# Optimization experiments

Hardware: AMD Instinct MI355X
Metric: run time of the kernel (lower is better)

## Reference

```python
import jax, jax.numpy as jnp
import numpy as np

POOL = (7, 7)


def crop_and_resize(image, boxes, box_idx, crop_size):
    """Faithful jnp port of tf.image.crop_and_resize (bilinear, extrapolation_value=0).

    image: [B, H, W, C]; boxes: [N, 4] normalized (y1, x1, y2, x2); box_idx: [N] int.
    Returns [N, ph, pw, C].
    """
    H, W = image.shape[1], image.shape[2]
    ph, pw = crop_size
    y1, x1, y2, x2 = boxes[:, 0], boxes[:, 1], boxes[:, 2], boxes[:, 3]
    iy = jnp.arange(ph, dtype=image.dtype)
    ix = jnp.arange(pw, dtype=image.dtype)
    # sample coords in source-pixel space, TF convention for crop_size > 1
    ys = y1[:, None] * (H - 1) + iy[None, :] * ((y2 - y1)[:, None] * (H - 1) / (ph - 1))  # [N, ph]
    xs = x1[:, None] * (W - 1) + ix[None, :] * ((x2 - x1)[:, None] * (W - 1) / (pw - 1))  # [N, pw]
    vy = (ys >= 0) & (ys <= H - 1)
    vx = (xs >= 0) & (xs <= W - 1)
    y0 = jnp.floor(ys)
    x0 = jnp.floor(xs)
    wy = (ys - y0)[:, :, None, None]   # [N, ph, 1, 1]
    wx = (xs - x0)[:, None, :, None]   # [N, 1, pw, 1]
    y0i = jnp.clip(y0, 0, H - 1).astype(jnp.int32)
    y1i = jnp.clip(y0 + 1, 0, H - 1).astype(jnp.int32)  # when ys is integral, wy==0 so clamp is harmless
    x0i = jnp.clip(x0, 0, W - 1).astype(jnp.int32)
    x1i = jnp.clip(x0 + 1, 0, W - 1).astype(jnp.int32)
    b = box_idx[:, None, None]

    def g(yi, xi):
        return image[b, yi[:, :, None], xi[:, None, :], :]  # [N, ph, pw, C]

    top = g(y0i, x0i) * (1 - wx) + g(y0i, x1i) * wx
    bot = g(y1i, x0i) * (1 - wx) + g(y1i, x1i) * wx
    out = top * (1 - wy) + bot * wy
    valid = (vy[:, :, None] & vx[:, None, :])[..., None]
    return jnp.where(valid, out, jnp.zeros((), image.dtype))


def setup_inputs() -> dict:
    key = jax.random.key(0)
    kb, kp, k3, k4, k5 = jax.random.split(key, 5)
    B, N, C = 2, 1000, 256
    # valid normalized boxes: per-axis sorted uniforms -> y1 <= y2, x1 <= x2
    raw = jax.random.uniform(kb, (B, N, 2, 2), dtype=jnp.float32)  # [..., (y|x), (lo,hi)]
    raw = jnp.sort(raw, axis=-1)
    boxes = jnp.stack([raw[..., 0, 0], raw[..., 1, 0], raw[..., 0, 1], raw[..., 1, 1]], axis=-1)
    return {
        "boxes": boxes,
        "positive_indices": jax.random.randint(kp, (B, N), 0, 2, dtype=jnp.int32),
        "p3": jax.random.normal(k3, (B, 128, 128, C), dtype=jnp.float32),
        "p4": jax.random.normal(k4, (B, 64, 64, C), dtype=jnp.float32),
        "p5": jax.random.normal(k5, (B, 32, 32, C), dtype=jnp.float32),
        "config": 0,
    }


def reference(boxes, positive_indices, p3, p4, p5, config):
    B, N = boxes.shape[0], boxes.shape[1]
    ph, pw = POOL
    h = boxes[..., 2] - boxes[..., 0]
    w = boxes[..., 3] - boxes[..., 1]
    # roi_level = clip(ceil(5 + log2(h*w)), 3, 5); clip in float first (log2(0) -> -inf)
    lvl = jnp.ceil(5.0 + jnp.log(h * w) / jnp.log(2.0))
    roi_level = jnp.clip(lvl, 3.0, 5.0).astype(jnp.int32)  # [B, N]
    boxes_flat = jax.lax.stop_gradient(boxes.reshape(B * N, 4))  # boxes get no grad in original
    lvl_flat = roi_level.reshape(B * N)
    box_idx = jnp.repeat(jnp.arange(B, dtype=jnp.int32), N)
    C = p3.shape[-1]
    pooled = jnp.zeros((B * N, ph, pw, C), dtype=p3.dtype)
    for level, feat in zip((3, 4, 5), (p3, p4, p5)):
        crop = crop_and_resize(feat, boxes_flat, box_idx, POOL)
        mask = (lvl_flat == level)[:, None, None, None]
        pooled = jnp.where(mask, crop, pooled)
    return pooled.reshape(B, N, ph, pw, C)
```

## Files before the change

kernel.cpp:

```cpp
#include <hip/hip_runtime.h>
#include <math.h>


#define NBOX   2000
#define N_PER_B 1000
#define CCH    256
#define PH     7
#define PW     7
#define NPOS   (PH * PW)

__global__ __launch_bounds__(256) void pyramid_roi_align_kernel(
    const float* __restrict__ boxes,
    const float* __restrict__ p3,
    const float* __restrict__ p4,
    const float* __restrict__ p5,
    float* __restrict__ out)
{
    const int tid  = blockIdx.x * blockDim.x + threadIdx.x;
    const int lane = threadIdx.x & 63;
    const int gpos = tid >> 6;
    if (gpos >= NBOX * NPOS) return;

    const int box = gpos / NPOS;
    const int pos = gpos - box * NPOS;
    const int iy  = pos / PW;
    const int ix  = pos - iy * PW;

    const float y1 = boxes[box * 4 + 0];
    const float x1 = boxes[box * 4 + 1];
    const float y2 = boxes[box * 4 + 2];
    const float x2 = boxes[box * 4 + 3];
    const float h  = y2 - y1;
    const float w  = x2 - x1;

    const float lvl = ceilf(5.0f + logf(h * w) / 0.69314718055994530942f);
    const float lvlc = fminf(fmaxf(lvl, 3.0f), 5.0f);
    const int level = (int)lvlc;

    const float* feat;
    int H;
    if (level <= 3)      { feat = p3; H = 128; }
    else if (level == 4) { feat = p4; H = 64;  }
    else                 { feat = p5; H = 32;  }
    const int W = H;

    const int b = (box >= N_PER_B) ? 1 : 0;
    feat += (size_t)b * H * W * CCH;

    const float Hm1 = (float)(H - 1);
    const float Wm1 = (float)(W - 1);

    const float ys = y1 * Hm1 + (float)iy * (h * Hm1 / 6.0f);
    const float xs = x1 * Wm1 + (float)ix * (w * Wm1 / 6.0f);

    const bool vy = (ys >= 0.0f) && (ys <= Hm1);
    const bool vx = (xs >= 0.0f) && (xs <= Wm1);
    const bool valid = vy && vx;

    const float y0f = floorf(ys);
    const float x0f = floorf(xs);
    const float wy  = ys - y0f;
    const float wx  = xs - x0f;

    const int y0i = (int)fminf(fmaxf(y0f,        0.0f), Hm1);
    const int y1i = (int)fminf(fmaxf(y0f + 1.0f, 0.0f), Hm1);
    const int x0i = (int)fminf(fmaxf(x0f,        0.0f), Wm1);
    const int x1i = (int)fminf(fmaxf(x0f + 1.0f, 0.0f), Wm1);

    const int c = lane * 4;
    const float4* r00 = (const float4*)(feat + ((size_t)(y0i * W + x0i)) * CCH + c);
    const float4* r01 = (const float4*)(feat + ((size_t)(y0i * W + x1i)) * CCH + c);
    const float4* r10 = (const float4*)(feat + ((size_t)(y1i * W + x0i)) * CCH + c);
    const float4* r11 = (const float4*)(feat + ((size_t)(y1i * W + x1i)) * CCH + c);

    const float4 v00 = *r00;
    const float4 v01 = *r01;
    const float4 v10 = *r10;
    const float4 v11 = *r11;

    const float omwx = 1.0f - wx;
    const float omwy = 1.0f - wy;

    float4 res;
    {
        const float t0 = v00.x * omwx + v01.x * wx;
        const float b0 = v10.x * omwx + v11.x * wx;
        res.x = t0 * omwy + b0 * wy;
        const float t1 = v00.y * omwx + v01.y * wx;
        const float b1 = v10.y * omwx + v11.y * wx;
        res.y = t1 * omwy + b1 * wy;
        const float t2 = v00.z * omwx + v01.z * wx;
        const float b2 = v10.z * omwx + v11.z * wx;
        res.z = t2 * omwy + b2 * wy;
        const float t3 = v00.w * omwx + v01.w * wx;
        const float b3 = v10.w * omwx + v11.w * wx;
        res.w = t3 * omwy + b3 * wy;
    }

    if (!valid) { res.x = 0.0f; res.y = 0.0f; res.z = 0.0f; res.w = 0.0f; }

    float4* dst = (float4*)(out + (size_t)gpos * CCH + c);
    *dst = res;
}

extern "C" void kernel_launch(void* const* d_in, const int* in_sizes, int n_in,
                              void* d_out, int out_size, void* d_ws, size_t ws_size,
                              hipStream_t stream) {
    const float* boxes = (const float*)d_in[0];
    const float* p3 = (const float*)d_in[2];
    const float* p4 = (const float*)d_in[3];
    const float* p5 = (const float*)d_in[4];
    float* out = (float*)d_out;

    const int total_threads = NBOX * NPOS * 64;
    const int block = 256;
    const int grid = (total_threads + block - 1) / block;

    hipLaunchKernelGGL(pyramid_roi_align_kernel, dim3(grid), dim3(block), 0, stream,
                       boxes, p3, p4, p5, out);
}
```

Baseline: 171.8 us.

## Map one block per box and loop output columns within each wavefront

The kernel now launches one 448-thread block per box, with each of the 7 wavefronts handling one output row and looping over the 7 columns. Box loading, level selection and the row-dependent interpolation terms are computed once per row instead of once per output position. The cost is fewer, longer-running threads and a serial unrolled loop over columns. Occupancy depends on register use under the new launch bounds.

```diff
diff --git a/kernel.cpp b/kernel.cpp
--- a/kernel.cpp
+++ b/kernel.cpp
@@ -2,29 +2,23 @@
 #include <math.h>
 
 
-#define NBOX   2000
 #define N_PER_B 1000
-#define CCH    256
-#define PH     7
-#define PW     7
-#define NPOS   (PH * PW)
+#define NBOX    2000
+#define CCH     256
+#define PH      7
+#define PW      7
 
-__global__ __launch_bounds__(256) void pyramid_roi_align_kernel(
+__global__ __launch_bounds__(448, 4) void pyramid_roi_align_kernel(
     const float* __restrict__ boxes,
     const float* __restrict__ p3,
     const float* __restrict__ p4,
     const float* __restrict__ p5,
     float* __restrict__ out)
 {
-    const int tid  = blockIdx.x * blockDim.x + threadIdx.x;
+    const int box  = blockIdx.x;
+    const int iy   = threadIdx.x >> 6;
     const int lane = threadIdx.x & 63;
-    const int gpos = tid >> 6;
-    if (gpos >= NBOX * NPOS) return;
-
-    const int box = gpos / NPOS;
-    const int pos = gpos - box * NPOS;
-    const int iy  = pos / PW;
-    const int ix  = pos - iy * PW;
+    const int c    = lane * 4;
 
     const float y1 = boxes[box * 4 + 0];
     const float x1 = boxes[box * 4 + 1];
@@ -33,9 +27,9 @@
     const float h  = y2 - y1;
     const float w  = x2 - x1;
 
-    const float lvl = ceilf(5.0f + logf(h * w) / 0.69314718055994530942f);
+    const float lvl  = ceilf(5.0f + logf(h * w) / 0.69314718055994530942f);
     const float lvlc = fminf(fmaxf(lvl, 3.0f), 5.0f);
-    const int level = (int)lvlc;
+    const int level  = (int)lvlc;
 
     const float* feat;
     int H;
@@ -51,56 +45,48 @@
     const float Wm1 = (float)(W - 1);
 
     const float ys = y1 * Hm1 + (float)iy * (h * Hm1 / 6.0f);
-    const float xs = x1 * Wm1 + (float)ix * (w * Wm1 / 6.0f);
-
-    const bool vy = (ys >= 0.0f) && (ys <= Hm1);
-    const bool vx = (xs >= 0.0f) && (xs <= Wm1);
-    const bool valid = vy && vx;
+    const bool  vy = (ys >= 0.0f) && (ys <= Hm1);
 
     const float y0f = floorf(ys);
-    const float x0f = floorf(xs);
     const float wy  = ys - y0f;
-    const float wx  = xs - x0f;
+    const float omwy = 1.0f - wy;
 
     const int y0i = (int)fminf(fmaxf(y0f,        0.0f), Hm1);
     const int y1i = (int)fminf(fmaxf(y0f + 1.0f, 0.0f), Hm1);
-    const int x0i = (int)fminf(fmaxf(x0f,        0.0f), Wm1);
-    const int x1i = (int)fminf(fmaxf(x0f + 1.0f, 0.0f), Wm1);
 
-    const int c = lane * 4;
-    const float4* r00 = (const float4*)(feat + ((size_t)(y0i * W + x0i)) * CCH + c);
-    const float4* r01 = (const float4*)(feat + ((size_t)(y0i * W + x1i)) * CCH + c);
-    const float4* r10 = (const float4*)(feat + ((size_t)(y1i * W + x0i)) * CCH + c);
-    const float4* r11 = (const float4*)(feat + ((size_t)(y1i * W + x1i)) * CCH + c);
+    const float* row0 = feat + (size_t)y0i * W * CCH + c;
+    const float* row1 = feat + (size_t)y1i * W * CCH + c;
 
-    const float4 v00 = *r00;
-    const float4 v01 = *r01;
-    const float4 v10 = *r10;
-    const float4 v11 = *r11;
+    const float xstep = w * Wm1 / 6.0f;
+    float* dst_base = out + ((size_t)box * (PH * PW) + (size_t)iy * PW) * CCH + c;
 
-    const float omwx = 1.0f - wx;
-    const float omwy = 1.0f - wy;
+#pragma unroll
+    for (int ix = 0; ix < PW; ++ix) {
+        const float xs = x1 * Wm1 + (float)ix * xstep;
+        const bool  vx = (xs >= 0.0f) && (xs <= Wm1);
 
-    float4 res;
-    {
-        const float t0 = v00.x * omwx + v01.x * wx;
-        const float b0 = v10.x * omwx + v11.x * wx;
-        res.x = t0 * omwy + b0 * wy;
-        const float t1 = v00.y * omwx + v01.y * wx;
-        const float b1 = v10.y * omwx + v11.y * wx;
-        res.y = t1 * omwy + b1 * wy;
-        const float t2 = v00.z * omwx + v01.z * wx;
-        const float b2 = v10.z * omwx + v11.z * wx;
-        res.z = t2 * omwy + b2 * wy;
-        const float t3 = v00.w * omwx + v01.w * wx;
-        const float b3 = v10.w * omwx + v11.w * wx;
-        res.w = t3 * omwy + b3 * wy;
+        const float x0f = floorf(xs);
+        const float wx  = xs - x0f;
+        const float omwx = 1.0f - wx;
+
+        const int x0i = (int)fminf(fmaxf(x0f,        0.0f), Wm1);
+        const int x1i = (int)fminf(fmaxf(x0f + 1.0f, 0.0f), Wm1);
+
+        const float4 v00 = *(const float4*)(row0 + (size_t)x0i * CCH);
+        const float4 v01 = *(const float4*)(row0 + (size_t)x1i * CCH);
+        const float4 v10 = *(const float4*)(row1 + (size_t)x0i * CCH);
+        const float4 v11 = *(const float4*)(row1 + (size_t)x1i * CCH);
+
+        float4 res;
+        res.x = (v00.x * omwx + v01.x * wx) * omwy + (v10.x * omwx + v11.x * wx) * wy;
+        res.y = (v00.y * omwx + v01.y * wx) * omwy + (v10.y * omwx + v11.y * wx) * wy;
+        res.z = (v00.z * omwx + v01.z * wx) * omwy + (v10.z * omwx + v11.z * wx) * wy;
+        res.w = (v00.w * omwx + v01.w * wx) * omwy + (v10.w * omwx + v11.w * wx) * wy;
+
+        if (!(vy && vx)) { res.x = 0.0f; res.y = 0.0f; res.z = 0.0f; res.w = 0.0f; }
+
+        *(float4*)(dst_base + (size_t)ix * CCH) = res;
     }
-
-    if (!valid) { res.x = 0.0f; res.y = 0.0f; res.z = 0.0f; res.w = 0.0f; }
-
-    float4* dst = (float4*)(out + (size_t)gpos * CCH + c);
-    *dst = res;
 }
 
 extern "C" void kernel_launch(void* const* d_in, const int* in_sizes, int n_in,
@@ -112,10 +98,6 @@
     const float* p5 = (const float*)d_in[4];
     float* out = (float*)d_out;
 
-    const int total_threads = NBOX * NPOS * 64;
-    const int block = 256;
-    const int grid = (total_threads + block - 1) / block;
-
-    hipLaunchKernelGGL(pyramid_roi_align_kernel, dim3(grid), dim3(block), 0, stream,
+    hipLaunchKernelGGL(pyramid_roi_align_kernel, dim3(NBOX), dim3(448), 0, stream,
                        boxes, p3, p4, p5, out);
 }
```

New measurement: 168.9 us. No clear change (-1.7%).
